# Kernel tuning notes

Hardware: AMD Instinct MI355X
Metric: run time of the kernel (lower is better)

The kernel has to match this reference:

```python
import jax, jax.numpy as jnp
import numpy as np

EPS = 1e-6  # T5LayerNorm epsilon


def setup_inputs() -> dict:
    key = jax.random.key(0)
    k0, k1, k2, k3 = jax.random.split(key, 4)
    B, S, D, F, E = 4, 2048, 768, 3072, 8
    hidden_states = jax.random.normal(k0, (B, S, D), jnp.float32)
    router_w = jax.random.normal(k1, (E, D), jnp.float32) * 0.02
    ln_w = jnp.ones((E, D), jnp.float32)
    wi = jax.random.normal(k2, (E, F, D), jnp.float32) * 0.02
    wo = jax.random.normal(k3, (E, D, F), jnp.float32) * 0.02
    return {"hidden_states": hidden_states, "router_w": router_w, "ln_w": ln_w,
            "wi": wi, "wo": wo, "top_k": 2}


def reference(hidden_states, router_w, ln_w, wi, wo, top_k):
    B, S, D = hidden_states.shape
    E = router_w.shape[0]
    x = hidden_states.reshape(-1, D)                      # [T, D] tokens
    router_logits = x @ router_w.T                        # [T, E]
    probs = jax.nn.softmax(router_logits, axis=-1)
    rw, sel = jax.lax.top_k(probs, top_k)                 # [T, K]
    rw = rw / jnp.sum(rw, axis=-1, keepdims=True)         # renormalize top-k weights

    # T5LayerNorm is RMS-norm (no mean subtraction); shared input x, per-expert scale.
    var = jnp.mean(x * x, axis=-1, keepdims=True)         # [T, 1]
    x_norm = x * jax.lax.rsqrt(var + EPS)                 # [T, D]

    out = jnp.zeros_like(x)
    for e in range(E):  # fixed small loop over experts (structurally distinct params)
        # combine weight for expert e: zero for tokens that did not select it
        w_e = jnp.sum(jnp.where(sel == e, rw, 0.0), axis=-1)   # [T]
        h = x_norm * ln_w[e]                                   # [T, D]
        ff = jax.nn.relu(h @ wi[e].T) @ wo[e].T                # [T, D]
        # T5LayerFF returns x + FFN(LN(x)); routing weight scales the whole output
        out = out + w_e[:, None] * (x + ff)
    layer_output = out.reshape(B, S, D)
    return layer_output, router_logits
```

## Files before the change

### kernel.cpp

```cpp
#include <hip/hip_runtime.h>
#include <hip/hip_bf16.h>
#include <math.h>

typedef short short8 __attribute__((ext_vector_type(8)));
typedef float f32x16 __attribute__((ext_vector_type(16)));

constexpr int D = 768;
constexpr int E = 8;
constexpr int F = 3072;
constexpr int FH = 1536;
constexpr int T = 8192;
constexpr float EPS = 1e-6f;

static __device__ inline unsigned short f2bf(float f) {
    __hip_bfloat16 h = __float2bfloat16(f);
    return *reinterpret_cast<unsigned short*>(&h);
}

static __device__ inline f32x16 mfma_bf16(short8 a, short8 b, f32x16 c) {
    return __builtin_amdgcn_mfma_f32_32x32x16_bf16(a, b, c, 0, 0, 0);
}

#define GLL16(g, s) __builtin_amdgcn_global_load_lds( \
    (const __attribute__((address_space(1))) unsigned int*)(g), \
    (__attribute__((address_space(3))) unsigned int*)(s), 16, 0, 0)

__global__ __launch_bounds__(256)
void convert_weights(const float* __restrict__ wi, const float* __restrict__ wo,
                     const float* __restrict__ lnw,
                     unsigned short* __restrict__ wip, unsigned short* __restrict__ wop)
{
    const unsigned NWI = (unsigned)E * F * D;
    unsigned i4 = (blockIdx.x * 256u + threadIdx.x) * 4u;
    if (i4 < NWI) {
        float4 v = *(const float4*)(wi + i4);
        unsigned e = i4 / (unsigned)(F * D);
        unsigned d = i4 % (unsigned)D;
        float4 l = *(const float4*)(lnw + e * D + d);
        ushort4 o = { f2bf(v.x * l.x), f2bf(v.y * l.y), f2bf(v.z * l.z), f2bf(v.w * l.w) };
        *(ushort4*)(wip + i4) = o;
    } else {
        unsigned j = i4 - NWI;
        float4 v = *(const float4*)(wo + j);
        ushort4 o = { f2bf(v.x), f2bf(v.y), f2bf(v.z), f2bf(v.w) };
        *(ushort4*)(wop + j) = o;
    }
}

__global__ __launch_bounds__(256)
void router_norm_kernel(const float* __restrict__ x,
                        const float* __restrict__ rw,
                        float* __restrict__ logits,
                        unsigned short* __restrict__ xn,
                        float* __restrict__ out,
                        int*   __restrict__ sel,
                        float2* __restrict__ w01)
{
    const int lane = threadIdx.x & 63;
    const int wid  = threadIdx.x >> 6;
    const int t = blockIdx.x * 4 + wid;
    if (t >= T) return;

    const float* xr = x + (size_t)t * D;
    float xv[12];
    float acc[8];
#pragma unroll
    for (int e = 0; e < 8; ++e) acc[e] = 0.f;
    float ssq = 0.f;
#pragma unroll
    for (int i = 0; i < 12; ++i) {
        const int k = lane + 64 * i;
        const float v = xr[k];
        xv[i] = v;
        ssq += v * v;
#pragma unroll
        for (int e = 0; e < 8; ++e) acc[e] += v * rw[e * D + k];
    }
#pragma unroll
    for (int off = 32; off; off >>= 1) {
        ssq += __shfl_xor(ssq, off);
#pragma unroll
        for (int e = 0; e < 8; ++e) acc[e] += __shfl_xor(acc[e], off);
    }

    int e0 = 0; float m0 = acc[0];
#pragma unroll
    for (int e = 1; e < 8; ++e) if (acc[e] > m0) { m0 = acc[e]; e0 = e; }
    int e1 = -1; float m1 = -3.4e38f;
#pragma unroll
    for (int e = 0; e < 8; ++e) if (e != e0 && acc[e] > m1) { m1 = acc[e]; e1 = e; }

    const float r  = expf(m1 - m0);
    const float w0 = 1.f / (1.f + r);
    const float w1 = r * w0;
    const float wsum = w0 + w1;
    const float rs = rsqrtf(ssq * (1.f / (float)D) + EPS);

    if (lane == 0) {
#pragma unroll
        for (int e = 0; e < 8; ++e) logits[t * 8 + e] = acc[e];
        sel[t] = e0 | (e1 << 4);
        w01[t] = make_float2(w0, w1);
    }

#pragma unroll
    for (int i = 0; i < 12; ++i) {
        const int k = lane + 64 * i;
        xn[(size_t)t * D + k] = f2bf(xv[i] * rs);
        out[(size_t)t * D + k] = wsum * xv[i];
    }
}

__global__ __launch_bounds__(256)
void build_lists(const int* __restrict__ sel, const float2* __restrict__ w01,
                 int* __restrict__ counts, int* __restrict__ lists,
                 float* __restrict__ wlist)
{
    const int e = blockIdx.x;
    const int tid = threadIdx.x;
    const int lane = tid & 63;
    const int wv = tid >> 6;
    __shared__ int wtot[4];
    int cnt = 0;
    for (int c0 = 0; c0 < T; c0 += 256) {
        const int t = c0 + tid;
        const int s = sel[t];
        const bool m1 = ((s >> 4) & 15) == e;
        const bool m = ((s & 15) == e) || m1;
        const unsigned long long b = __ballot(m);
        const int pre = __popcll(b & ((1ULL << lane) - 1ULL));
        if (lane == 0) wtot[wv] = __popcll(b);
        __syncthreads();
        int wbase = 0;
#pragma unroll
        for (int i = 0; i < 4; ++i) if (i < wv) wbase += wtot[i];
        if (m) {
            const int pos = cnt + wbase + pre;
            lists[e * T + pos] = (t << 1) | (m1 ? 1 : 0);
            const float2 w = w01[t];
            wlist[e * T + pos] = m1 ? w.y : w.x;
        }
        cnt += wtot[0] + wtot[1] + wtot[2] + wtot[3];
        __syncthreads();
    }
    if (tid == 0) counts[e] = cnt;
}

__global__ __launch_bounds__(256)
void gemm1_kernel(const unsigned short* __restrict__ xn,
                  const unsigned short* __restrict__ wip,
                  const int* __restrict__ counts,
                  const int* __restrict__ lists,
                  unsigned short* __restrict__ H, int half)
{
    __shared__ unsigned short sA[128 * 64];
    __shared__ unsigned short sB[128 * 64];
    __shared__ int s_tok[128];

    const int bid = blockIdx.x;
    const int e  = bid & 7;
    const int mt = (bid >> 3) / 12;
    const int nt = (bid >> 3) % 12;
    const int cnt = counts[e];
    const int base = mt * 128;
    if (base >= cnt) return;
    int offe = 0;
    for (int i = 0; i < e; ++i) offe += counts[i];

    const int tid = threadIdx.x;
    const int w = tid >> 6, l = tid & 63;
    const int lo = l & 31, hi = l >> 5;
    const int wr = w >> 1, wc = w & 1;

    if (tid < 128) {
        const int idx = base + tid;
        s_tok[tid] = (idx < cnt) ? (lists[e * T + idx] >> 1) : 0;
    }
    __syncthreads();

    const int r = (w * 4 + 0) * 8 + (l >> 3);
    const int chS = ((l & 7) ^ ((l >> 3) & 7)) * 8;
    const unsigned short* aSrc[4];
    const unsigned short* bSrc[4];
#pragma unroll
    for (int j = 0; j < 4; ++j) {
        const int rj = r + j * 8;
        aSrc[j] = xn + (size_t)s_tok[rj] * D + chS;
        bSrc[j] = wip + ((size_t)e * F + half * FH + nt * 128 + rj) * D + chS;
    }
    char* sAc = (char*)sA;
    char* sBc = (char*)sB;

    f32x16 acc00, acc01, acc10, acc11;
#pragma unroll
    for (int q = 0; q < 16; ++q) { acc00[q] = 0.f; acc01[q] = 0.f; acc10[q] = 0.f; acc11[q] = 0.f; }

    const int rx = (lo & 7) << 4;
    const int arow0 = (wr * 64 + lo) * 128;
    const int arow1 = arow0 + 32 * 128;
    const int brow0 = (wc * 64 + lo) * 128;
    const int brow1 = brow0 + 32 * 128;

    for (int kt = 0; kt < 12; ++kt) {
        const int k0 = kt * 64;
#pragma unroll
        for (int j = 0; j < 4; ++j) {
            GLL16(aSrc[j] + k0, sAc + (w * 4 + j) * 1024);
            GLL16(bSrc[j] + k0, sBc + (w * 4 + j) * 1024);
        }
        __syncthreads();
#pragma unroll
        for (int ks = 0; ks < 4; ++ks) {
            const int coff = (hi * 16 + ks * 32) ^ rx;
            short8 a0 = *(const short8*)(sAc + arow0 + coff);
            short8 a1 = *(const short8*)(sAc + arow1 + coff);
            short8 b0 = *(const short8*)(sBc + brow0 + coff);
            short8 b1 = *(const short8*)(sBc + brow1 + coff);
            acc00 = mfma_bf16(a0, b0, acc00);
            acc01 = mfma_bf16(a0, b1, acc01);
            acc10 = mfma_bf16(a1, b0, acc10);
            acc11 = mfma_bf16(a1, b1, acc11);
        }
        __syncthreads();
    }

    const int cbase = nt * 128 + wc * 64 + lo;
#pragma unroll
    for (int rr = 0; rr < 16; ++rr) {
        const int crow = (rr & 3) + 8 * (rr >> 2) + 4 * hi;
        int lrow = wr * 64 + crow;
        if (base + lrow < cnt) {
            unsigned short* hp = H + (size_t)(offe + base + lrow) * FH + cbase;
            hp[0]  = f2bf(fmaxf(acc00[rr], 0.f));
            hp[32] = f2bf(fmaxf(acc01[rr], 0.f));
        }
        lrow += 32;
        if (base + lrow < cnt) {
            unsigned short* hp = H + (size_t)(offe + base + lrow) * FH + cbase;
            hp[0]  = f2bf(fmaxf(acc10[rr], 0.f));
            hp[32] = f2bf(fmaxf(acc11[rr], 0.f));
        }
    }
}

__global__ __launch_bounds__(256)
void gemm2_kernel(const unsigned short* __restrict__ H,
                  const unsigned short* __restrict__ wop,
                  const int* __restrict__ counts,
                  const int* __restrict__ lists, const float* __restrict__ wlist,
                  float* __restrict__ out, float* __restrict__ ffout,
                  int half, int mode)
{
    __shared__ unsigned short sA[128 * 64];
    __shared__ unsigned short sB[128 * 64];
    __shared__ int   s_tok[128];
    __shared__ float s_wgt[128];

    const int bid = blockIdx.x;
    const int e  = bid & 7;
    const int mt = (bid >> 3) / 6;
    const int nt = (bid >> 3) % 6;
    const int cnt = counts[e];
    const int base = mt * 128;
    if (base >= cnt) return;
    int offe = 0;
    for (int i = 0; i < e; ++i) offe += counts[i];

    const int tid = threadIdx.x;
    const int w = tid >> 6, l = tid & 63;
    const int lo = l & 31, hi = l >> 5;
    const int wr = w >> 1, wc = w & 1;

    if (tid < 128) {
        const int idx = base + tid;
        const bool v = idx < cnt;
        s_tok[tid] = v ? lists[e * T + idx] : 0;
        s_wgt[tid] = v ? wlist[e * T + idx] : 0.f;
    }

    const int r = (w * 4 + 0) * 8 + (l >> 3);
    const int chS = ((l & 7) ^ ((l >> 3) & 7)) * 8;
    const unsigned short* aSrc[4];
    const unsigned short* bSrc[4];
#pragma unroll
    for (int j = 0; j < 4; ++j) {
        const int rj = r + j * 8;
        aSrc[j] = H + (size_t)(offe + base + rj) * FH + chS;
        bSrc[j] = wop + ((size_t)e * D + nt * 128 + rj) * F + half * FH + chS;
    }
    char* sAc = (char*)sA;
    char* sBc = (char*)sB;

    f32x16 acc00, acc01, acc10, acc11;
#pragma unroll
    for (int q = 0; q < 16; ++q) { acc00[q] = 0.f; acc01[q] = 0.f; acc10[q] = 0.f; acc11[q] = 0.f; }

    const int rx = (lo & 7) << 4;
    const int arow0 = (wr * 64 + lo) * 128;
    const int arow1 = arow0 + 32 * 128;
    const int brow0 = (wc * 64 + lo) * 128;
    const int brow1 = brow0 + 32 * 128;

    for (int kt = 0; kt < 24; ++kt) {
        const int k0 = kt * 64;
#pragma unroll
        for (int j = 0; j < 4; ++j) {
            GLL16(aSrc[j] + k0, sAc + (w * 4 + j) * 1024);
            GLL16(bSrc[j] + k0, sBc + (w * 4 + j) * 1024);
        }
        __syncthreads();
#pragma unroll
        for (int ks = 0; ks < 4; ++ks) {
            const int coff = (hi * 16 + ks * 32) ^ rx;
            short8 a0 = *(const short8*)(sAc + arow0 + coff);
            short8 a1 = *(const short8*)(sAc + arow1 + coff);
            short8 b0 = *(const short8*)(sBc + brow0 + coff);
            short8 b1 = *(const short8*)(sBc + brow1 + coff);
            acc00 = mfma_bf16(a0, b0, acc00);
            acc01 = mfma_bf16(a0, b1, acc01);
            acc10 = mfma_bf16(a1, b0, acc10);
            acc11 = mfma_bf16(a1, b1, acc11);
        }
        __syncthreads();
    }

    const int cbase = nt * 128 + wc * 64 + lo;
#pragma unroll
    for (int rr = 0; rr < 16; ++rr) {
        const int crow = (rr & 3) + 8 * (rr >> 2) + 4 * hi;
#pragma unroll
        for (int mh = 0; mh < 2; ++mh) {
            const int lrow = wr * 64 + crow + mh * 32;
            if (base + lrow < cnt) {
                const int pk = s_tok[lrow];
                const float wgt = s_wgt[lrow];
                const float v0 = wgt * (mh ? acc10[rr] : acc00[rr]);
                const float v1 = wgt * (mh ? acc11[rr] : acc01[rr]);
                if (mode == 0) {
                    float* dst = out + (size_t)(pk >> 1) * D + cbase;
                    atomicAdd(dst,      v0);
                    atomicAdd(dst + 32, v1);
                } else {
                    float* dst = ffout + ((size_t)(pk & 1) * T + (pk >> 1)) * D + cbase;
                    if (mode == 1) { dst[0] = v0;  dst[32] = v1; }
                    else           { dst[0] += v0; dst[32] += v1; }
                }
            }
        }
    }
}

__global__ __launch_bounds__(256)
void combine_kernel(const float* __restrict__ ffout, float* __restrict__ out)
{
    const long long i4 = ((long long)blockIdx.x * 256 + threadIdx.x) * 4;
    float4 o  = *(const float4*)(out + i4);
    float4 f0 = *(const float4*)(ffout + i4);
    float4 f1 = *(const float4*)(ffout + (long long)T * D + i4);
    o.x += f0.x + f1.x; o.y += f0.y + f1.y;
    o.z += f0.z + f1.z; o.w += f0.w + f1.w;
    *(float4*)(out + i4) = o;
}

extern "C" void kernel_launch(void* const* d_in, const int* in_sizes, int n_in,
                              void* d_out, int out_size, void* d_ws, size_t ws_size,
                              hipStream_t stream) {
    const float* x   = (const float*)d_in[0];
    const float* rw  = (const float*)d_in[1];
    const float* lnw = (const float*)d_in[2];
    const float* wi  = (const float*)d_in[3];
    const float* wo  = (const float*)d_in[4];

    float* out    = (float*)d_out;
    float* logits = (float*)d_out + (size_t)T * D;

    char* ws = (char*)d_ws;
    int*            counts = (int*)(ws);
    int*            sel    = (int*)(ws + 4096);
    float2*         w01    = (float2*)(ws + 65536);
    int*            lists  = (int*)(ws + 131072);
    float*          wlist  = (float*)(ws + 393216);
    unsigned short* xn     = (unsigned short*)(ws + 1048576);
    unsigned short* wip    = (unsigned short*)(ws + 13631488);
    unsigned short* wop    = (unsigned short*)(ws + 51380224);
    unsigned short* H      = (unsigned short*)(ws + 89128960);
    float*          ffout  = (float*)(ws + 140247040);

    const bool big = ws_size >= 190578688ULL;

    convert_weights<<<36864, 256, 0, stream>>>(wi, wo, lnw, wip, wop);

    router_norm_kernel<<<T / 4, 256, 0, stream>>>(x, rw, logits, xn, out,
                                                  sel, w01);

    build_lists<<<E, 256, 0, stream>>>(sel, w01, counts, lists, wlist);

    for (int h = 0; h < 2; ++h) {
        gemm1_kernel<<<32 * 12 * 8, 256, 0, stream>>>(xn, wip, counts,
                                                      lists, H, h);
        const int mode = big ? (h ? 2 : 1) : 0;
        gemm2_kernel<<<32 * 6 * 8, 256, 0, stream>>>(H, wop, counts,
                                                     lists, wlist, out,
                                                     ffout, h, mode);
    }

    if (big) combine_kernel<<<T * D / 4 / 256, 256, 0, stream>>>(ffout, out);
}
```

Before: 363.9 us.

## Double-buffer LDS tiles with async prefetch two stages ahead in expert GEMMs

Replaces the single-buffer load/sync/compute loop in both expert GEMM kernels with a two-stage LDS ring. Global-to-LDS loads for tile k+2 are issued right after the fragments of tile k are read into registers, so memory latency overlaps the MFMA work. Explicit vmcnt/lgkmcnt waits and sched barriers order the steps. LDS use per block grows to 64KB, which may reduce occupancy, and the last iterations re-issue redundant loads of the final tile.

```diff
diff --git a/kernel.cpp b/kernel.cpp
--- a/kernel.cpp
+++ b/kernel.cpp
@@ -146,6 +146,59 @@
     if (tid == 0) counts[e] = cnt;
 }
 
+
+#define GEMM_PIPE_LOOP(NKT)                                                   \
+           \
+    _Pragma("unroll")                                                         \
+    for (int j = 0; j < 4; ++j) {                                             \
+        GLL16(aSrc[j], smem + stg + j * 1024);                                \
+        GLL16(bSrc[j], smem + 16384 + stg + j * 1024);                        \
+    }                                                                         \
+    _Pragma("unroll")                                                         \
+    for (int j = 0; j < 4; ++j) {                                             \
+        GLL16(aSrc[j] + 64, smem + 32768 + stg + j * 1024);                   \
+        GLL16(bSrc[j] + 64, smem + 32768 + 16384 + stg + j * 1024);           \
+    }                                                                         \
+    asm volatile("s_waitcnt vmcnt(8)" ::: "memory");                          \
+    __builtin_amdgcn_s_barrier();                                             \
+    int cur = 0;                                                              \
+    for (int kt = 0; kt < (NKT); ++kt) {                                      \
+        const char* cA = smem + cur * 32768;                                  \
+        const char* cB = cA + 16384;                                          \
+        short8 fA0[4], fA1[4], fB0[4], fB1[4];                                \
+        _Pragma("unroll")                                                     \
+        for (int ks = 0; ks < 4; ++ks) {                                      \
+            const int coff = (hi * 16 + ks * 32) ^ rx;                        \
+            fA0[ks] = *(const short8*)(cA + arow0 + coff);                    \
+            fA1[ks] = *(const short8*)(cA + arow1 + coff);                    \
+            fB0[ks] = *(const short8*)(cB + brow0 + coff);                    \
+            fB1[ks] = *(const short8*)(cB + brow1 + coff);                    \
+        }                                                                     \
+        asm volatile("s_waitcnt lgkmcnt(0)" ::: "memory");                    \
+        __builtin_amdgcn_sched_barrier(0);                                    \
+        __builtin_amdgcn_s_barrier();    \
+        {                                                                     \
+            const int kn = (kt + 2 < (NKT) ? kt + 2 : (NKT)-1) * 64;          \
+            char* dA = smem + cur * 32768;                                    \
+            _Pragma("unroll")                                                 \
+            for (int j = 0; j < 4; ++j) {                                     \
+                GLL16(aSrc[j] + kn, dA + stg + j * 1024);                     \
+                GLL16(bSrc[j] + kn, dA + 16384 + stg + j * 1024);             \
+            }                                                                 \
+        }                                                                     \
+        __builtin_amdgcn_sched_barrier(0);                                    \
+        _Pragma("unroll")                                                     \
+        for (int ks = 0; ks < 4; ++ks) {                                      \
+            acc00 = mfma_bf16(fA0[ks], fB0[ks], acc00);                       \
+            acc01 = mfma_bf16(fA0[ks], fB1[ks], acc01);                       \
+            acc10 = mfma_bf16(fA1[ks], fB0[ks], acc10);                       \
+            acc11 = mfma_bf16(fA1[ks], fB1[ks], acc11);                       \
+        }                                                                     \
+        asm volatile("s_waitcnt vmcnt(8)" ::: "memory");                      \
+        __builtin_amdgcn_s_barrier();    \
+        cur ^= 1;                                                             \
+    }
+
 __global__ __launch_bounds__(256)
 void gemm1_kernel(const unsigned short* __restrict__ xn,
                   const unsigned short* __restrict__ wip,
@@ -153,8 +206,7 @@
                   const int* __restrict__ lists,
                   unsigned short* __restrict__ H, int half)
 {
-    __shared__ unsigned short sA[128 * 64];
-    __shared__ unsigned short sB[128 * 64];
+    __shared__ __align__(16) char smem[65536];
     __shared__ int s_tok[128];
 
     const int bid = blockIdx.x;
@@ -188,8 +240,6 @@
         aSrc[j] = xn + (size_t)s_tok[rj] * D + chS;
         bSrc[j] = wip + ((size_t)e * F + half * FH + nt * 128 + rj) * D + chS;
     }
-    char* sAc = (char*)sA;
-    char* sBc = (char*)sB;
 
     f32x16 acc00, acc01, acc10, acc11;
 #pragma unroll
@@ -200,29 +250,9 @@
     const int arow1 = arow0 + 32 * 128;
     const int brow0 = (wc * 64 + lo) * 128;
     const int brow1 = brow0 + 32 * 128;
-
-    for (int kt = 0; kt < 12; ++kt) {
-        const int k0 = kt * 64;
-#pragma unroll
-        for (int j = 0; j < 4; ++j) {
-            GLL16(aSrc[j] + k0, sAc + (w * 4 + j) * 1024);
-            GLL16(bSrc[j] + k0, sBc + (w * 4 + j) * 1024);
-        }
-        __syncthreads();
-#pragma unroll
-        for (int ks = 0; ks < 4; ++ks) {
-            const int coff = (hi * 16 + ks * 32) ^ rx;
-            short8 a0 = *(const short8*)(sAc + arow0 + coff);
-            short8 a1 = *(const short8*)(sAc + arow1 + coff);
-            short8 b0 = *(const short8*)(sBc + brow0 + coff);
-            short8 b1 = *(const short8*)(sBc + brow1 + coff);
-            acc00 = mfma_bf16(a0, b0, acc00);
-            acc01 = mfma_bf16(a0, b1, acc01);
-            acc10 = mfma_bf16(a1, b0, acc10);
-            acc11 = mfma_bf16(a1, b1, acc11);
-        }
-        __syncthreads();
-    }
+    const int stg = w * 4096;
+
+    GEMM_PIPE_LOOP(12)
 
     const int cbase = nt * 128 + wc * 64 + lo;
 #pragma unroll
@@ -251,8 +281,7 @@
                   float* __restrict__ out, float* __restrict__ ffout,
                   int half, int mode)
 {
-    __shared__ unsigned short sA[128 * 64];
-    __shared__ unsigned short sB[128 * 64];
+    __shared__ __align__(16) char smem[65536];
     __shared__ int   s_tok[128];
     __shared__ float s_wgt[128];
 
@@ -277,6 +306,7 @@
         s_tok[tid] = v ? lists[e * T + idx] : 0;
         s_wgt[tid] = v ? wlist[e * T + idx] : 0.f;
     }
+    __syncthreads();
 
     const int r = (w * 4 + 0) * 8 + (l >> 3);
     const int chS = ((l & 7) ^ ((l >> 3) & 7)) * 8;
@@ -288,8 +318,6 @@
         aSrc[j] = H + (size_t)(offe + base + rj) * FH + chS;
         bSrc[j] = wop + ((size_t)e * D + nt * 128 + rj) * F + half * FH + chS;
     }
-    char* sAc = (char*)sA;
-    char* sBc = (char*)sB;
 
     f32x16 acc00, acc01, acc10, acc11;
 #pragma unroll
@@ -300,29 +328,9 @@
     const int arow1 = arow0 + 32 * 128;
     const int brow0 = (wc * 64 + lo) * 128;
     const int brow1 = brow0 + 32 * 128;
-
-    for (int kt = 0; kt < 24; ++kt) {
-        const int k0 = kt * 64;
-#pragma unroll
-        for (int j = 0; j < 4; ++j) {
-            GLL16(aSrc[j] + k0, sAc + (w * 4 + j) * 1024);
-            GLL16(bSrc[j] + k0, sBc + (w * 4 + j) * 1024);
-        }
-        __syncthreads();
-#pragma unroll
-        for (int ks = 0; ks < 4; ++ks) {
-            const int coff = (hi * 16 + ks * 32) ^ rx;
-            short8 a0 = *(const short8*)(sAc + arow0 + coff);
-            short8 a1 = *(const short8*)(sAc + arow1 + coff);
-            short8 b0 = *(const short8*)(sBc + brow0 + coff);
-            short8 b1 = *(const short8*)(sBc + brow1 + coff);
-            acc00 = mfma_bf16(a0, b0, acc00);
-            acc01 = mfma_bf16(a0, b1, acc01);
-            acc10 = mfma_bf16(a1, b0, acc10);
-            acc11 = mfma_bf16(a1, b1, acc11);
-        }
-        __syncthreads();
-    }
+    const int stg = w * 4096;
+
+    GEMM_PIPE_LOOP(24)
 
     const int cbase = nt * 128 + wc * 64 + lo;
 #pragma unroll
```

Result: no change. 360.1 us (-1.0%).

## Merge F halves into single GEMM launches with split-K atomics and compact lists

Applied to the files above, without the earlier changes.

The FFN previously ran as two passes over half of F. Each pass had its own gemm1/gemm2 launch, and partial outputs went to a scratch buffer that a final combine kernel summed. Now gemm1 computes the full F width in one launch, and gemm2 splits K into two halves inside one grid, accumulating into the output with atomics. List building becomes count, prefix and place kernels that produce compact per-expert offsets, and gemm2 gains a barrier before the shared token list is read. This removes the combine pass, the scratch traffic and extra launches, but makes every output write an atomic add.

```diff
diff --git a/kernel.cpp b/kernel.cpp
--- a/kernel.cpp
+++ b/kernel.cpp
@@ -8,7 +8,6 @@
 constexpr int D = 768;
 constexpr int E = 8;
 constexpr int F = 3072;
-constexpr int FH = 1536;
 constexpr int T = 8192;
 constexpr float EPS = 1e-6f;
 
@@ -112,11 +111,40 @@
 }
 
 __global__ __launch_bounds__(256)
-void build_lists(const int* __restrict__ sel, const float2* __restrict__ w01,
-                 int* __restrict__ counts, int* __restrict__ lists,
-                 float* __restrict__ wlist)
+void count_kernel(const int* __restrict__ sel, int* __restrict__ counts)
 {
     const int e = blockIdx.x;
+    const int tid = threadIdx.x;
+    int c = 0;
+    for (int t = tid; t < T; t += 256) {
+        const int s = sel[t];
+        c += ((s & 15) == e) + (((s >> 4) & 15) == e);
+    }
+#pragma unroll
+    for (int off = 32; off; off >>= 1) c += __shfl_xor(c, off);
+    __shared__ int ws4[4];
+    if ((tid & 63) == 0) ws4[tid >> 6] = c;
+    __syncthreads();
+    if (tid == 0) counts[e] = ws4[0] + ws4[1] + ws4[2] + ws4[3];
+}
+
+__global__ void prefix_kernel(const int* __restrict__ counts, int* __restrict__ offs)
+{
+    if (threadIdx.x == 0 && blockIdx.x == 0) {
+        int a = 0;
+#pragma unroll
+        for (int e = 0; e < 8; ++e) { offs[e] = a; a += counts[e]; }
+        offs[8] = a;
+    }
+}
+
+__global__ __launch_bounds__(256)
+void place_kernel(const int* __restrict__ sel, const float2* __restrict__ w01,
+                  const int* __restrict__ offs,
+                  int* __restrict__ lists, float* __restrict__ wlist)
+{
+    const int e = blockIdx.x;
+    const int base = offs[e];
     const int tid = threadIdx.x;
     const int lane = tid & 63;
     const int wv = tid >> 6;
@@ -135,23 +163,23 @@
 #pragma unroll
         for (int i = 0; i < 4; ++i) if (i < wv) wbase += wtot[i];
         if (m) {
-            const int pos = cnt + wbase + pre;
-            lists[e * T + pos] = (t << 1) | (m1 ? 1 : 0);
+            const int pos = base + cnt + wbase + pre;
+            lists[pos] = (t << 1) | (m1 ? 1 : 0);
             const float2 w = w01[t];
-            wlist[e * T + pos] = m1 ? w.y : w.x;
+            wlist[pos] = m1 ? w.y : w.x;
         }
         cnt += wtot[0] + wtot[1] + wtot[2] + wtot[3];
         __syncthreads();
     }
-    if (tid == 0) counts[e] = cnt;
-}
+}
+
 
 __global__ __launch_bounds__(256)
 void gemm1_kernel(const unsigned short* __restrict__ xn,
                   const unsigned short* __restrict__ wip,
-                  const int* __restrict__ counts,
+                  const int* __restrict__ offs,
                   const int* __restrict__ lists,
-                  unsigned short* __restrict__ H, int half)
+                  unsigned short* __restrict__ H)
 {
     __shared__ unsigned short sA[128 * 64];
     __shared__ unsigned short sB[128 * 64];
@@ -159,13 +187,13 @@
 
     const int bid = blockIdx.x;
     const int e  = bid & 7;
-    const int mt = (bid >> 3) / 12;
-    const int nt = (bid >> 3) % 12;
-    const int cnt = counts[e];
+    const int q  = bid >> 3;
+    const int mt = q / 24;
+    const int nt = q % 24;
+    const int offe = offs[e];
+    const int cnt = offs[e + 1] - offe;
     const int base = mt * 128;
     if (base >= cnt) return;
-    int offe = 0;
-    for (int i = 0; i < e; ++i) offe += counts[i];
 
     const int tid = threadIdx.x;
     const int w = tid >> 6, l = tid & 63;
@@ -174,7 +202,7 @@
 
     if (tid < 128) {
         const int idx = base + tid;
-        s_tok[tid] = (idx < cnt) ? (lists[e * T + idx] >> 1) : 0;
+        s_tok[tid] = (idx < cnt) ? (lists[offe + idx] >> 1) : 0;
     }
     __syncthreads();
 
@@ -186,14 +214,14 @@
     for (int j = 0; j < 4; ++j) {
         const int rj = r + j * 8;
         aSrc[j] = xn + (size_t)s_tok[rj] * D + chS;
-        bSrc[j] = wip + ((size_t)e * F + half * FH + nt * 128 + rj) * D + chS;
+        bSrc[j] = wip + ((size_t)e * F + nt * 128 + rj) * D + chS;
     }
     char* sAc = (char*)sA;
     char* sBc = (char*)sB;
 
     f32x16 acc00, acc01, acc10, acc11;
 #pragma unroll
-    for (int q = 0; q < 16; ++q) { acc00[q] = 0.f; acc01[q] = 0.f; acc10[q] = 0.f; acc11[q] = 0.f; }
+    for (int qq = 0; qq < 16; ++qq) { acc00[qq] = 0.f; acc01[qq] = 0.f; acc10[qq] = 0.f; acc11[qq] = 0.f; }
 
     const int rx = (lo & 7) << 4;
     const int arow0 = (wr * 64 + lo) * 128;
@@ -230,13 +258,13 @@
         const int crow = (rr & 3) + 8 * (rr >> 2) + 4 * hi;
         int lrow = wr * 64 + crow;
         if (base + lrow < cnt) {
-            unsigned short* hp = H + (size_t)(offe + base + lrow) * FH + cbase;
+            unsigned short* hp = H + (size_t)(offe + base + lrow) * F + cbase;
             hp[0]  = f2bf(fmaxf(acc00[rr], 0.f));
             hp[32] = f2bf(fmaxf(acc01[rr], 0.f));
         }
         lrow += 32;
         if (base + lrow < cnt) {
-            unsigned short* hp = H + (size_t)(offe + base + lrow) * FH + cbase;
+            unsigned short* hp = H + (size_t)(offe + base + lrow) * F + cbase;
             hp[0]  = f2bf(fmaxf(acc10[rr], 0.f));
             hp[32] = f2bf(fmaxf(acc11[rr], 0.f));
         }
@@ -246,10 +274,9 @@
 __global__ __launch_bounds__(256)
 void gemm2_kernel(const unsigned short* __restrict__ H,
                   const unsigned short* __restrict__ wop,
-                  const int* __restrict__ counts,
+                  const int* __restrict__ offs,
                   const int* __restrict__ lists, const float* __restrict__ wlist,
-                  float* __restrict__ out, float* __restrict__ ffout,
-                  int half, int mode)
+                  float* __restrict__ out)
 {
     __shared__ unsigned short sA[128 * 64];
     __shared__ unsigned short sB[128 * 64];
@@ -258,13 +285,15 @@
 
     const int bid = blockIdx.x;
     const int e  = bid & 7;
-    const int mt = (bid >> 3) / 6;
-    const int nt = (bid >> 3) % 6;
-    const int cnt = counts[e];
+    const int q  = bid >> 3;
+    const int kh = q / 384;
+    const int rm = q % 384;
+    const int mt = rm / 6;
+    const int nt = rm % 6;
+    const int offe = offs[e];
+    const int cnt = offs[e + 1] - offe;
     const int base = mt * 128;
     if (base >= cnt) return;
-    int offe = 0;
-    for (int i = 0; i < e; ++i) offe += counts[i];
 
     const int tid = threadIdx.x;
     const int w = tid >> 6, l = tid & 63;
@@ -274,9 +303,10 @@
     if (tid < 128) {
         const int idx = base + tid;
         const bool v = idx < cnt;
-        s_tok[tid] = v ? lists[e * T + idx] : 0;
-        s_wgt[tid] = v ? wlist[e * T + idx] : 0.f;
-    }
+        s_tok[tid] = v ? lists[offe + idx] : 0;
+        s_wgt[tid] = v ? wlist[offe + idx] : 0.f;
+    }
+    __syncthreads();
 
     const int r = (w * 4 + 0) * 8 + (l >> 3);
     const int chS = ((l & 7) ^ ((l >> 3) & 7)) * 8;
@@ -285,15 +315,15 @@
 #pragma unroll
     for (int j = 0; j < 4; ++j) {
         const int rj = r + j * 8;
-        aSrc[j] = H + (size_t)(offe + base + rj) * FH + chS;
-        bSrc[j] = wop + ((size_t)e * D + nt * 128 + rj) * F + half * FH + chS;
+        aSrc[j] = H + (size_t)(offe + base + rj) * F + kh * 1536 + chS;
+        bSrc[j] = wop + ((size_t)e * D + nt * 128 + rj) * F + kh * 1536 + chS;
     }
     char* sAc = (char*)sA;
     char* sBc = (char*)sB;
 
     f32x16 acc00, acc01, acc10, acc11;
 #pragma unroll
-    for (int q = 0; q < 16; ++q) { acc00[q] = 0.f; acc01[q] = 0.f; acc10[q] = 0.f; acc11[q] = 0.f; }
+    for (int qq = 0; qq < 16; ++qq) { acc00[qq] = 0.f; acc01[qq] = 0.f; acc10[qq] = 0.f; acc11[qq] = 0.f; }
 
     const int rx = (lo & 7) << 4;
     const int arow0 = (wr * 64 + lo) * 128;
@@ -332,34 +362,14 @@
         for (int mh = 0; mh < 2; ++mh) {
             const int lrow = wr * 64 + crow + mh * 32;
             if (base + lrow < cnt) {
-                const int pk = s_tok[lrow];
+                const int tk = s_tok[lrow] >> 1;
                 const float wgt = s_wgt[lrow];
-                const float v0 = wgt * (mh ? acc10[rr] : acc00[rr]);
-                const float v1 = wgt * (mh ? acc11[rr] : acc01[rr]);
-                if (mode == 0) {
-                    float* dst = out + (size_t)(pk >> 1) * D + cbase;
-                    atomicAdd(dst,      v0);
-                    atomicAdd(dst + 32, v1);
-                } else {
-                    float* dst = ffout + ((size_t)(pk & 1) * T + (pk >> 1)) * D + cbase;
-                    if (mode == 1) { dst[0] = v0;  dst[32] = v1; }
-                    else           { dst[0] += v0; dst[32] += v1; }
-                }
+                float* dst = out + (size_t)tk * D + cbase;
+                atomicAdd(dst,      wgt * (mh ? acc10[rr] : acc00[rr]));
+                atomicAdd(dst + 32, wgt * (mh ? acc11[rr] : acc01[rr]));
             }
         }
     }
-}
-
-__global__ __launch_bounds__(256)
-void combine_kernel(const float* __restrict__ ffout, float* __restrict__ out)
-{
-    const long long i4 = ((long long)blockIdx.x * 256 + threadIdx.x) * 4;
-    float4 o  = *(const float4*)(out + i4);
-    float4 f0 = *(const float4*)(ffout + i4);
-    float4 f1 = *(const float4*)(ffout + (long long)T * D + i4);
-    o.x += f0.x + f1.x; o.y += f0.y + f1.y;
-    o.z += f0.z + f1.z; o.w += f0.w + f1.w;
-    *(float4*)(out + i4) = o;
 }
 
 extern "C" void kernel_launch(void* const* d_in, const int* in_sizes, int n_in,
@@ -375,34 +385,27 @@
     float* logits = (float*)d_out + (size_t)T * D;
 
     char* ws = (char*)d_ws;
-    int*            counts = (int*)(ws);
-    int*            sel    = (int*)(ws + 4096);
-    float2*         w01    = (float2*)(ws + 65536);
-    int*            lists  = (int*)(ws + 131072);
-    float*          wlist  = (float*)(ws + 393216);
-    unsigned short* xn     = (unsigned short*)(ws + 1048576);
-    unsigned short* wip    = (unsigned short*)(ws + 13631488);
-    unsigned short* wop    = (unsigned short*)(ws + 51380224);
-    unsigned short* H      = (unsigned short*)(ws + 89128960);
-    float*          ffout  = (float*)(ws + 140247040);
-
-    const bool big = ws_size >= 190578688ULL;
+    unsigned short* xn     = (unsigned short*)(ws);
+    unsigned short* wip    = (unsigned short*)(ws + 12582912);
+    unsigned short* wop    = (unsigned short*)(ws + 50331648);
+    unsigned short* H      = (unsigned short*)(ws + 88080384);
+    int*            counts = (int*)(ws + 190316544);
+    int*            offs   = (int*)(ws + 190316608);
+    int*            sel    = (int*)(ws + 190316672);
+    float2*         w01    = (float2*)(ws + 190349440);
+    int*            lists  = (int*)(ws + 190414976);
+    float*          wlist  = (float*)(ws + 190480512);
 
     convert_weights<<<36864, 256, 0, stream>>>(wi, wo, lnw, wip, wop);
 
     router_norm_kernel<<<T / 4, 256, 0, stream>>>(x, rw, logits, xn, out,
                                                   sel, w01);
 
-    build_lists<<<E, 256, 0, stream>>>(sel, w01, counts, lists, wlist);
-
-    for (int h = 0; h < 2; ++h) {
-        gemm1_kernel<<<32 * 12 * 8, 256, 0, stream>>>(xn, wip, counts,
-                                                      lists, H, h);
-        const int mode = big ? (h ? 2 : 1) : 0;
-        gemm2_kernel<<<32 * 6 * 8, 256, 0, stream>>>(H, wop, counts,
-                                                     lists, wlist, out,
-                                                     ffout, h, mode);
-    }
-
-    if (big) combine_kernel<<<T * D / 4 / 256, 256, 0, stream>>>(ffout, out);
-}
+    count_kernel<<<E, 256, 0, stream>>>(sel, counts);
+    prefix_kernel<<<1, 1, 0, stream>>>(counts, offs);
+    place_kernel<<<E, 256, 0, stream>>>(sel, w01, offs, lists, wlist);
+
+    gemm1_kernel<<<64 * 24 * 8, 256, 0, stream>>>(xn, wip, offs, lists, H);
+    gemm2_kernel<<<2 * 64 * 6 * 8, 256, 0, stream>>>(H, wop, offs, lists,
+                                                     wlist, out);
+}
```

After: 332.1 us. 8.7% less time.
